# Kernel tuning notes

Measured on AMD Instinct MI355X. Metric: run time of the kernel, lower is better.

Reference implementation:

```python
import jax, jax.numpy as jnp
import numpy as np

NE, NT, NC, D, NR = 100000, 1024, 128, 128, 500
H, E, L_GCN = 8, 4, 2
B, DEG = 512, 8
NSRC = B * DEG
NNZ_E2T, NNZ_T2C, NNZ_E2C = 1000000, 50000, 500000
TAU, DECAY, CLW = 0.5, 1e-4, 0.1
N_NODES = NE + NT + NC


def setup_inputs() -> dict:
    ks = iter(jax.random.split(jax.random.key(0), 64))
    def n(shape, s=0.05):
        return jax.random.normal(next(ks), shape, jnp.float32) * s
    def ri(shape, hi):
        return jax.random.randint(next(ks), shape, 0, hi, jnp.int32)
    def u(shape):
        return jax.random.uniform(next(ks), shape, jnp.float32) * 0.01
    T = NT
    return {
        'entity_emb': n((NE, D)), 'type_emb': n((NT, D)), 'cluster_emb': n((NC, D)),
        'relation': n((NR, 2 * D)),
        'ln_g': jnp.ones((D,), jnp.float32), 'ln_b': jnp.zeros((D,), jnp.float32),
        'cl_w1': n((D, D)), 'cl_b1': jnp.zeros((D,), jnp.float32),
        'cl_w2': n((D, D)), 'cl_b2': jnp.zeros((D,), jnp.float32),
        'fc_w': n((2 * D, T)), 'fc_b': jnp.zeros((T,), jnp.float32),
        'wq': n((T, T)), 'bq': jnp.zeros((T,), jnp.float32),
        'wk': n((T, T)), 'bk': jnp.zeros((T,), jnp.float32),
        'wv': n((T, T)), 'bv': jnp.zeros((T,), jnp.float32),
        'wo': n((T, T)), 'bo': jnp.zeros((T,), jnp.float32),
        'gate_w': n((T, E)), 'exp_w': n((E, T, T)), 'exp_b': jnp.zeros((E, T), jnp.float32),
        'e2t_val': u((NNZ_E2T,)), 't2c_val': u((NNZ_T2C,)), 'e2c_val': u((NNZ_E2C,)),
        'e2t_row': ri((NNZ_E2T,), NE + NT), 'e2t_col': ri((NNZ_E2T,), NE + NT),
        't2c_row': ri((NNZ_T2C,), NT + NC), 't2c_col': ri((NNZ_T2C,), NT + NC),
        'e2c_row': ri((NNZ_E2C,), NE + NC), 'e2c_col': ri((NNZ_E2C,), NE + NC),
        'src_ids': ri((NSRC,), N_NODES), 'etype': ri((NSRC,), 2 * NR),
    }


def _light_gcn(ea, eb, row, col, val, na, nb):
    x = jnp.concatenate([ea, eb], axis=0)
    acc = x
    for _ in range(L_GCN):  # fixed small layer count
        x = jax.ops.segment_sum(val[:, None] * x[col], row, num_segments=na + nb)
        acc = acc + x
    m = acc / (L_GCN + 1)
    return m[:na], m[na:]


def _ln(x, g, b):
    mu = x.mean(-1, keepdims=True)
    var = x.var(-1, keepdims=True)
    return (x - mu) * jax.lax.rsqrt(var + 1e-5) * g + b


def _cl_loss(src1, src2, w1, b1, w2, b2):
    def proj(x):
        return jax.nn.elu(x @ w1 + b1) @ w2 + b2
    def norm(x):
        return x / jnp.maximum(jnp.linalg.norm(x, axis=1, keepdims=True), 1e-12)
    z1, z2 = norm(proj(src1)), norm(proj(src2))
    s11 = jnp.exp(z1 @ z1.T / TAU)   # [N,N]
    s12 = jnp.exp(z1 @ z2.T / TAU)
    s22 = jnp.exp(z2 @ z2.T / TAU)
    d12 = jnp.diag(s12)
    l1 = -jnp.log(d12 / (s11.sum(1) + s12.sum(1) - jnp.diag(s11)))
    l2 = -jnp.log(d12 / (s22.sum(1) + s12.sum(0) - jnp.diag(s22)))
    return ((l1 + l2) * 0.5).mean()


def _mha_moe(x, wq, bq, wk, bk, wv, bv, wo, bo, gate_w, exp_w, exp_b):
    # x: [B, DEG, T]; MHA over mailbox axis, then softmax-gated MoE, mean-pool.
    b, l, t = x.shape
    dh = t // H
    q = (x @ wq + bq).reshape(b, l, H, dh)
    k = (x @ wk + bk).reshape(b, l, H, dh)
    v = (x @ wv + bv).reshape(b, l, H, dh)
    attn = jax.nn.softmax(jnp.einsum('blhd,bmhd->bhlm', q, k) / jnp.sqrt(jnp.float32(dh)), axis=-1)
    o = jnp.einsum('bhlm,bmhd->blhd', attn, v).reshape(b, l, t) @ wo + bo
    gate = jax.nn.softmax(o @ gate_w, axis=-1)               # [B,L,E]
    eo = jnp.einsum('blt,etu->bleu', o, exp_w) + exp_b       # [B,L,E,T]
    moe = jnp.einsum('ble,blet->blt', gate, eo)
    return moe.mean(axis=1)                                  # [B,T]


def reference(entity_emb, type_emb, cluster_emb, relation, ln_g, ln_b,
              cl_w1, cl_b1, cl_w2, cl_b2, fc_w, fc_b,
              wq, bq, wk, bk, wv, bv, wo, bo, gate_w, exp_w, exp_b,
              e2t_val, t2c_val, e2c_val,
              e2t_row, e2t_col, t2c_row, t2c_col, e2c_row, e2c_col,
              src_ids, etype):
    e2t_e, e2t_t = _light_gcn(entity_emb, type_emb, e2t_row, e2t_col, e2t_val, NE, NT)
    t2c_t, t2c_c = _light_gcn(type_emb, cluster_emb, t2c_row, t2c_col, t2c_val, NT, NC)
    e2c_e, e2c_c = _light_gcn(entity_emb, cluster_emb, e2c_row, e2c_col, e2c_val, NE, NC)
    # with_norm=True path; dropout is eval-mode identity
    e2t_e, e2t_t = _ln(e2t_e, ln_g, ln_b), _ln(e2t_t, ln_g, ln_b)
    t2c_t, t2c_c = _ln(t2c_t, ln_g, ln_b), _ln(t2c_c, ln_g, ln_b)
    e2c_e, e2c_c = _ln(e2c_e, ln_g, ln_b), _ln(e2c_c, ln_g, ln_b)
    node1 = jnp.concatenate([e2t_e, e2t_t, t2c_c], axis=0)
    node2 = jnp.concatenate([e2c_e, t2c_t, e2c_c], axis=0)
    src1 = node1[src_ids]   # [NSRC, D]
    src2 = node2[src_ids]
    cl = _cl_loss(src1, src2, cl_w1, cl_b1, cl_w2, cl_b2)
    src = jnp.concatenate([src1, src2], axis=-1)  # [NSRC, 2D]
    sign = jnp.where(etype >= NR, -1.0, 1.0).astype(jnp.float32)[:, None]
    rel = relation[etype % NR] * sign
    emb_loss = DECAY * ((src ** 2).sum() + (rel ** 2).sum()) * 0.5 / rel.shape[0]
    aux_loss = CLW * cl + emb_loss
    # update_all: u_add_e message, regular mailbox [B, DEG, 2D]
    msg = jax.nn.relu(src + rel).reshape(B, DEG, 2 * D)
    predict = msg @ fc_w + fc_b                                  # [B, DEG, NT]
    predict = _mha_moe(predict, wq, bq, wk, bk, wv, bv, wo, bo, gate_w, exp_w, exp_b)
    out = jax.nn.sigmoid(predict)                                # [B, NT]
    return out, aux_loss
```

## Files before the change

### kernel.cpp

```cpp
#include <hip/hip_runtime.h>
#include <hip/hip_bf16.h>
#include <cmath>

constexpr int cNE = 100000, cNT = 1024, cNC = 128, cD = 128, cNR = 500;
constexpr int cB = 512, cNSRC = 4096, cT = 1024, cE = 4;
constexpr int cNNZ_E2T = 1000000, cNNZ_T2C = 50000, cNNZ_E2C = 500000;
constexpr float cDECAY = 1e-4f, cCLW = 0.1f;
constexpr int cNN_E2T = cNE + cNT;
constexpr int cNN_E2C = cNE + cNC;
constexpr int cNN_T2C = cNT + cNC;

constexpr size_t F_S1   = 0;
constexpr size_t F_S2   = F_S1 + 524288;
constexpr size_t F_PT   = F_S2 + 524288;
constexpr size_t F_Z1   = F_PT + 524288;
constexpr size_t F_Z2   = F_Z1 + 524288;
constexpr size_t F_MSG  = F_Z2 + 524288;
constexpr size_t F_GATE = F_MSG + 524288;
constexpr size_t F_SCAL = F_GATE + 16384;
constexpr size_t F_RS   = F_SCAL + 64;
constexpr size_t F_D11  = F_RS + 16384;
constexpr size_t F_D12  = F_D11 + 4096;
constexpr size_t F_D22  = F_D12 + 4096;
constexpr size_t F_U    = F_D22 + 4096;
constexpr size_t G_X1F  = F_U;
constexpr size_t G_X2C  = G_X1F + 6465536;
constexpr size_t G_SLOT = G_X2C + 262144;
constexpr size_t G_REP  = G_SLOT + 101376;
constexpr size_t G_RP   = G_REP + 4096;
constexpr size_t G_FILL = G_RP + 101376;
constexpr size_t G_COLS = G_FILL + 101376;
constexpr size_t G_VALS = G_COLS + 1000000;
constexpr size_t G_X1T  = G_VALS + 1000000;
constexpr size_t G_X2T  = G_X1T + 73728;
constexpr size_t G_BSUM = G_X2T + 73728;
constexpr size_t G_EBF  = G_BSUM + 512;
constexpr size_t G_TBF  = G_EBF + 3200000;
constexpr size_t G_CBF  = G_TBF + 65536;
constexpr size_t A_U0  = F_U;
constexpr size_t A_U1  = F_U + 2097152;
constexpr size_t A_WBT = F_U + 4 * 2097152;

typedef __attribute__((ext_vector_type(8))) short short8v;
typedef __attribute__((ext_vector_type(4))) float f32x4;

__device__ __forceinline__ void atomAdd(float* p, float v) {
  __hip_atomic_fetch_add(p, v, __ATOMIC_RELAXED, __HIP_MEMORY_SCOPE_AGENT);
}
__device__ __forceinline__ ushort f2bf(float f) {
  __hip_bfloat16 h = __float2bfloat16(f);
  return *reinterpret_cast<ushort*>(&h);
}
__device__ __forceinline__ float bf2f(ushort u) {
  __hip_bfloat16 h; *reinterpret_cast<ushort*>(&h) = u;
  return __bfloat162float(h);
}

__device__ __forceinline__ int mapNode(int mode, int id) {
  switch (mode) {
    case 0:  return (id < cNE + cNT) ? id : -1;
    case 1:  return (id >= cNE + cNT) ? (id - cNE) : -1;
    case 2:  return (id >= cNE && id < cNE + cNT) ? (id - cNE) : -1;
    default: return (id < cNE) ? id
                   : ((id >= cNE + cNT) ? (id - cNT) : -1);
  }
}

__device__ __forceinline__ float blockReduce256(float v, float* sh, int tid) {
  sh[tid] = v; __syncthreads();
  for (int s = 128; s > 0; s >>= 1) {
    if (tid < s) sh[tid] += sh[tid + s];
    __syncthreads();
  }
  float r = sh[0]; __syncthreads();
  return r;
}

__global__ __launch_bounds__(256) void k_to_bf(const float* __restrict__ src,
                                               ushort* __restrict__ dst, int nq) {
  for (int q = blockIdx.x * 256 + threadIdx.x; q < nq; q += gridDim.x * 256) {
    float4 v = *reinterpret_cast<const float4*>(src + (size_t)q * 4);
    ushort4 o;
    o.x = f2bf(v.x); o.y = f2bf(v.y); o.z = f2bf(v.z); o.w = f2bf(v.w);
    *reinterpret_cast<ushort4*>(dst + (size_t)q * 4) = o;
  }
}

__global__ __launch_bounds__(256) void k_pack_bias(const float* __restrict__ b0,
                                                   const float* __restrict__ b1,
                                                   const float* __restrict__ b2,
                                                   float* __restrict__ dst) {
  int i = blockIdx.x * 256 + threadIdx.x;
  float v = (i < 1024) ? b0[i] : (i < 2048) ? b1[i - 1024] : b2[i - 2048];
  dst[i] = v;
}

__global__ __launch_bounds__(256) void k_init3(int* __restrict__ slot, int* __restrict__ mark,
                                               int* __restrict__ fill, int n) {
  int i = blockIdx.x * 256 + threadIdx.x;
  if (i < n) { slot[i] = 0x7f7f7f7f; mark[i] = 0; fill[i] = 0; }
}

__global__ __launch_bounds__(256) void k_slot_mark(const int* __restrict__ ids,
                                                   int* __restrict__ slot,
                                                   int* __restrict__ mark, int mode) {
  int i = blockIdx.x * 256 + threadIdx.x;
  if (i >= cNSRC) return;
  int node = mapNode(mode, ids[i]);
  if (node >= 0) { atomicMin(&slot[node], i); mark[node] = 1; }
}

__global__ __launch_bounds__(256) void k_mark_edges(const int* __restrict__ row,
                                                    const int* __restrict__ col, int nnz,
                                                    const int* __restrict__ slot,
                                                    int* __restrict__ mark) {
  int e = blockIdx.x * 256 + threadIdx.x;
  if (e >= nnz) return;
  int r = row[e];
  if (slot[r] < cNSRC) mark[col[e]] = 1;
}

__global__ __launch_bounds__(256) void k_hist(const int* __restrict__ row, int nnz,
                                              const int* __restrict__ mark,
                                              int* __restrict__ cnt) {
  int e = blockIdx.x * 256 + threadIdx.x;
  if (e >= nnz) return;
  int r = row[e];
  if (mark && !mark[r]) return;
  atomicAdd(&cnt[r], 1);
}

__global__ __launch_bounds__(256) void k_scan_block(const int* __restrict__ cnt, int n,
                                                    int* __restrict__ excl, int* __restrict__ bsum) {
  __shared__ int sh[256];
  int tid = threadIdx.x;
  int i = blockIdx.x * 256 + tid;
  int v = (i < n) ? cnt[i] : 0;
  sh[tid] = v; __syncthreads();
  for (int off = 1; off < 256; off <<= 1) {
    int t = (tid >= off) ? sh[tid - off] : 0;
    __syncthreads();
    sh[tid] += t;
    __syncthreads();
  }
  if (i < n) excl[i] = sh[tid] - v;
  if (tid == 255) bsum[blockIdx.x] = sh[255];
}

__global__ __launch_bounds__(512) void k_bsum_scan(int* __restrict__ bsum, int nb,
                                                   int* __restrict__ rowptr, int n) {
  __shared__ int sh[512];
  int tid = threadIdx.x;
  int v = (tid < nb) ? bsum[tid] : 0;
  sh[tid] = v; __syncthreads();
  for (int off = 1; off < 512; off <<= 1) {
    int t = (tid >= off) ? sh[tid - off] : 0;
    __syncthreads();
    sh[tid] += t;
    __syncthreads();
  }
  if (tid < nb) bsum[tid] = sh[tid] - v;
  if (tid == 511) rowptr[n] = sh[511];
}

__global__ __launch_bounds__(256) void k_scan_add(int* __restrict__ rowptr,
                                                  const int* __restrict__ bsum, int n,
                                                  int* __restrict__ fill) {
  int i = blockIdx.x * 256 + threadIdx.x;
  if (i < n) {
    int r = rowptr[i] + bsum[blockIdx.x];
    rowptr[i] = r;
    fill[i] = r;
  }
}

__global__ __launch_bounds__(256) void k_fill(const int* __restrict__ row,
                                              const int* __restrict__ col,
                                              const float* __restrict__ val, int nnz,
                                              const int* __restrict__ mark,
                                              int* __restrict__ fill,
                                              int* __restrict__ cols, float* __restrict__ vals) {
  int e = blockIdx.x * 256 + threadIdx.x;
  if (e >= nnz) return;
  int r = row[e];
  if (mark && !mark[r]) return;
  int pos = atomicAdd(&fill[r], 1);
  cols[pos] = col[e];
  vals[pos] = val[e];
}

__global__ __launch_bounds__(256) void k_gather(
    const int* __restrict__ rowptr, const int* __restrict__ cols, const float* __restrict__ vals,
    const ushort* __restrict__ ea, const ushort* __restrict__ eb, int na,
    int nrows, const int* __restrict__ mark, ushort* __restrict__ out) {
  int r = blockIdx.x * 4 + (threadIdx.x >> 6);
  if (r >= nrows) return;
  if (mark && !mark[r]) return;
  int lane = threadIdx.x & 63;
  int p0 = rowptr[r], p1 = rowptr[r + 1];
  float ax = 0.f, ay = 0.f;
  int p = p0;
  for (; p + 4 <= p1; p += 4) {
    int c0 = cols[p], c1 = cols[p + 1], c2 = cols[p + 2], c3 = cols[p + 3];
    float v0 = vals[p], v1 = vals[p + 1], v2 = vals[p + 2], v3 = vals[p + 3];
    const ushort* s0 = (c0 < na) ? (ea + (size_t)c0 * cD) : (eb + (size_t)(c0 - na) * cD);
    const ushort* s1 = (c1 < na) ? (ea + (size_t)c1 * cD) : (eb + (size_t)(c1 - na) * cD);
    const ushort* s2 = (c2 < na) ? (ea + (size_t)c2 * cD) : (eb + (size_t)(c2 - na) * cD);
    const ushort* s3 = (c3 < na) ? (ea + (size_t)c3 * cD) : (eb + (size_t)(c3 - na) * cD);
    ushort2 x0 = *reinterpret_cast<const ushort2*>(s0 + lane * 2);
    ushort2 x1 = *reinterpret_cast<const ushort2*>(s1 + lane * 2);
    ushort2 x2 = *reinterpret_cast<const ushort2*>(s2 + lane * 2);
    ushort2 x3 = *reinterpret_cast<const ushort2*>(s3 + lane * 2);
    ax += v0 * bf2f(x0.x) + v1 * bf2f(x1.x) + v2 * bf2f(x2.x) + v3 * bf2f(x3.x);
    ay += v0 * bf2f(x0.y) + v1 * bf2f(x1.y) + v2 * bf2f(x2.y) + v3 * bf2f(x3.y);
  }
  for (; p < p1; ++p) {
    int c = cols[p];
    float v = vals[p];
    const ushort* s = (c < na) ? (ea + (size_t)c * cD) : (eb + (size_t)(c - na) * cD);
    ushort2 x = *reinterpret_cast<const ushort2*>(s + lane * 2);
    ax += v * bf2f(x.x); ay += v * bf2f(x.y);
  }
  ushort2 o; o.x = f2bf(ax); o.y = f2bf(ay);
  *reinterpret_cast<ushort2*>(out + (size_t)r * cD + lane * 2) = o;
}

__global__ __launch_bounds__(256) void k_rep(const int* __restrict__ ids,
                                             const int* __restrict__ slot, int mode,
                                             int* __restrict__ rep) {
  int i = blockIdx.x * 256 + threadIdx.x;
  if (i >= cNSRC) return;
  int node = mapNode(mode, ids[i]);
  rep[i] = (node >= 0 && slot[node] == i) ? node : -1;
}

__global__ __launch_bounds__(256) void k_gather_slot(
    const int* __restrict__ rowptr, const int* __restrict__ cols, const float* __restrict__ vals,
    const ushort* __restrict__ x1, const int* __restrict__ rep,
    ushort* __restrict__ outc) {
  int i = blockIdx.x * 4 + (threadIdx.x >> 6);
  if (i >= cNSRC) return;
  int r = rep[i];
  if (r < 0) return;
  int lane = threadIdx.x & 63;
  int p0 = rowptr[r], p1 = rowptr[r + 1];
  float ax = 0.f, ay = 0.f;
  int p = p0;
  for (; p + 4 <= p1; p += 4) {
    int c0 = cols[p], c1 = cols[p + 1], c2 = cols[p + 2], c3 = cols[p + 3];
    float v0 = vals[p], v1 = vals[p + 1], v2 = vals[p + 2], v3 = vals[p + 3];
    ushort2 x0 = *reinterpret_cast<const ushort2*>(x1 + (size_t)c0 * cD + lane * 2);
    ushort2 x1v = *reinterpret_cast<const ushort2*>(x1 + (size_t)c1 * cD + lane * 2);
    ushort2 x2 = *reinterpret_cast<const ushort2*>(x1 + (size_t)c2 * cD + lane * 2);
    ushort2 x3 = *reinterpret_cast<const ushort2*>(x1 + (size_t)c3 * cD + lane * 2);
    ax += v0 * bf2f(x0.x) + v1 * bf2f(x1v.x) + v2 * bf2f(x2.x) + v3 * bf2f(x3.x);
    ay += v0 * bf2f(x0.y) + v1 * bf2f(x1v.y) + v2 * bf2f(x2.y) + v3 * bf2f(x3.y);
  }
  for (; p < p1; ++p) {
    int c = cols[p];
    float v = vals[p];
    ushort2 x = *reinterpret_cast<const ushort2*>(x1 + (size_t)c * cD + lane * 2);
    ax += v * bf2f(x.x); ay += v * bf2f(x.y);
  }
  ushort2 o; o.x = f2bf(ax); o.y = f2bf(ay);
  *reinterpret_cast<ushort2*>(outc + (size_t)i * cD + lane * 2) = o;
}

__global__ __launch_bounds__(256) void k_gather_bf(
    const int* __restrict__ rowptr, const int* __restrict__ cols, const float* __restrict__ vals,
    const ushort* __restrict__ x1, int nrows, ushort* __restrict__ out) {
  int r = blockIdx.x * 4 + (threadIdx.x >> 6);
  if (r >= nrows) return;
  int lane = threadIdx.x & 63;
  int p0 = rowptr[r], p1 = rowptr[r + 1];
  float ax = 0.f, ay = 0.f;
  for (int p = p0; p < p1; ++p) {
    int c = cols[p];
    float v = vals[p];
    ushort2 x = *reinterpret_cast<const ushort2*>(x1 + (size_t)c * cD + lane * 2);
    ax += v * bf2f(x.x); ay += v * bf2f(x.y);
  }
  ushort2 o; o.x = f2bf(ax); o.y = f2bf(ay);
  *reinterpret_cast<ushort2*>(out + (size_t)r * cD + lane * 2) = o;
}

__global__ __launch_bounds__(128) void gather_ln(
    const int* __restrict__ ids, int mode,
    const float* __restrict__ ea, const float* __restrict__ eb, int na,
    const ushort* __restrict__ x1, const ushort* __restrict__ x2, const int* __restrict__ slot,
    const float* __restrict__ g, const float* __restrict__ bia, float* __restrict__ dst) {
  __shared__ float shx[2], shy[2];
  int i = blockIdx.x;
  int tid = threadIdx.x;
  int id = ids[i];
  int node = mapNode(mode, id);
  if (node < 0) return;
  const float* x0 = (node < na) ? (ea + (size_t)node * cD) : (eb + (size_t)(node - na) * cD);
  int xi2 = slot ? slot[node] : node;
  float a = (x0[tid] + bf2f(x1[(size_t)node * cD + tid]) + bf2f(x2[(size_t)xi2 * cD + tid]))
            * (1.0f / 3.0f);
  float sx = a, sy = a * a;
#pragma unroll
  for (int off = 32; off > 0; off >>= 1) {
    sx += __shfl_xor(sx, off);
    sy += __shfl_xor(sy, off);
  }
  if ((tid & 63) == 0) { shx[tid >> 6] = sx; shy[tid >> 6] = sy; }
  __syncthreads();
  float s  = shx[0] + shx[1];
  float ss = shy[0] + shy[1];
  float mu = s * (1.0f / 128.0f);
  float var = ss * (1.0f / 128.0f) - mu * mu;
  float y = (a - mu) * rsqrtf(var + 1e-5f) * g[tid] + bia[tid];
  dst[(size_t)i * cD + tid] = y;
}

__global__ __launch_bounds__(256) void gemm_bf(
    const ushort* __restrict__ A, const ushort* __restrict__ Bt,
    int N, int K, const float* __restrict__ bias, ushort* __restrict__ Cbf, int epi) {
  __shared__ ushort As[128 * 40];
  __shared__ ushort Bs[128 * 40];
  const int bx = blockIdx.x, by = blockIdx.y;
  const int t = threadIdx.x;
  const int wv = t >> 6, lane = t & 63;
  const int wr = (wv >> 1) * 64, wc = (wv & 1) * 64;
  const int srow = t >> 1, shalf = t & 1;
  const ushort* Ag = A + (size_t)(by * 128 + srow) * K + shalf * 16;
  const ushort* Bg = Bt + (size_t)(bx * 128 + srow) * K + shalf * 16;
  uint4 ra0 = *reinterpret_cast<const uint4*>(Ag);
  uint4 ra1 = *reinterpret_cast<const uint4*>(Ag + 8);
  uint4 rb0 = *reinterpret_cast<const uint4*>(Bg);
  uint4 rb1 = *reinterpret_cast<const uint4*>(Bg + 8);
  f32x4 acc[4][4];
  const f32x4 z4 = {0.f, 0.f, 0.f, 0.f};
#pragma unroll
  for (int i = 0; i < 4; ++i)
#pragma unroll
    for (int j = 0; j < 4; ++j) acc[i][j] = z4;
  const int la = lane & 15, lk = (lane >> 4) * 8;
  const int sdst = srow * 40 + shalf * 16;
  for (int kt = 0; kt < K; kt += 32) {
    __syncthreads();
    *reinterpret_cast<uint4*>(&As[sdst])     = ra0;
    *reinterpret_cast<uint4*>(&As[sdst + 8]) = ra1;
    *reinterpret_cast<uint4*>(&Bs[sdst])     = rb0;
    *reinterpret_cast<uint4*>(&Bs[sdst + 8]) = rb1;
    __syncthreads();
    if (kt + 32 < K) {
      ra0 = *reinterpret_cast<const uint4*>(Ag + kt + 32);
      ra1 = *reinterpret_cast<const uint4*>(Ag + kt + 40);
      rb0 = *reinterpret_cast<const uint4*>(Bg + kt + 32);
      rb1 = *reinterpret_cast<const uint4*>(Bg + kt + 40);
    }
    short8v af[4], bfr[4];
#pragma unroll
    for (int i = 0; i < 4; ++i)
      af[i] = *reinterpret_cast<const short8v*>(&As[(wr + i * 16 + la) * 40 + lk]);
#pragma unroll
    for (int j = 0; j < 4; ++j)
      bfr[j] = *reinterpret_cast<const short8v*>(&Bs[(wc + j * 16 + la) * 40 + lk]);
#pragma unroll
    for (int i = 0; i < 4; ++i)
#pragma unroll
      for (int j = 0; j < 4; ++j)
        acc[i][j] = __builtin_amdgcn_mfma_f32_16x16x32_bf16(af[i], bfr[j], acc[i][j], 0, 0, 0);
  }
  const int r0 = by * 128 + wr + (lane >> 4) * 4;
  const int c0 = bx * 128 + wc + la;
#pragma unroll
  for (int i = 0; i < 4; ++i)
#pragma unroll
    for (int j = 0; j < 4; ++j) {
      int c = c0 + j * 16;
      float bv = bias[c];
#pragma unroll
      for (int q = 0; q < 4; ++q) {
        int r = r0 + i * 16 + q;
        float v = acc[i][j][q] + bv;
        if (epi == 1) v = (v > 0.0f) ? v : expm1f(v);
        Cbf[(size_t)r * N + c] = f2bf(v);
      }
    }
}

__global__ __launch_bounds__(256) void k_gate_pool(
    const ushort* __restrict__ o, const float* __restrict__ gw,
    ushort* __restrict__ ae, float* __restrict__ gsum) {
  __shared__ float os[8][1024];
  __shared__ float lg[8][4];
  __shared__ float gs[8][4];
  const int b = blockIdx.x, t = threadIdx.x;
  for (int u = t; u < 8192; u += 256) {
    int l = u >> 10, d = u & 1023;
    os[l][d] = bf2f(o[(size_t)(b * 8 + l) * 1024 + d]);
  }
  __syncthreads();
  {
    int p = t >> 3, sub = t & 7;
    int l = p >> 2, e = p & 3;
    float s = 0;
    for (int d = sub; d < 1024; d += 8) s += os[l][d] * gw[d * 4 + e];
    s += __shfl_down(s, 4, 8);
    s += __shfl_down(s, 2, 8);
    s += __shfl_down(s, 1, 8);
    if (sub == 0) lg[l][e] = s;
  }
  __syncthreads();
  if (t < 8) {
    float m = fmaxf(fmaxf(lg[t][0], lg[t][1]), fmaxf(lg[t][2], lg[t][3]));
    float e0 = expf(lg[t][0] - m), e1 = expf(lg[t][1] - m);
    float e2 = expf(lg[t][2] - m), e3 = expf(lg[t][3] - m);
    float inv = 1.0f / (e0 + e1 + e2 + e3);
    gs[t][0] = e0 * inv; gs[t][1] = e1 * inv;
    gs[t][2] = e2 * inv; gs[t][3] = e3 * inv;
  }
  __syncthreads();
  if (t < 4) {
    float g = 0;
#pragma unroll
    for (int l = 0; l < 8; ++l) g += gs[l][t];
    gsum[b * 4 + t] = g;
  }
#pragma unroll
  for (int rep = 0; rep < 4; ++rep) {
    int d = t + rep * 256;
    float a0 = 0, a1 = 0, a2 = 0, a3 = 0;
#pragma unroll
    for (int l = 0; l < 8; ++l) {
      float ov = os[l][d];
      a0 += gs[l][0] * ov; a1 += gs[l][1] * ov;
      a2 += gs[l][2] * ov; a3 += gs[l][3] * ov;
    }
    ae[(size_t)0 * 524288 + b * 1024 + d] = f2bf(a0);
    ae[(size_t)1 * 524288 + b * 1024 + d] = f2bf(a1);
    ae[(size_t)2 * 524288 + b * 1024 + d] = f2bf(a2);
    ae[(size_t)3 * 524288 + b * 1024 + d] = f2bf(a3);
  }
}

__global__ __launch_bounds__(256) void gemm_moe2(
    const ushort* __restrict__ AE, const ushort* __restrict__ Bt4,
    const float* __restrict__ expb, const float* __restrict__ gsum,
    float* __restrict__ out) {
  __shared__ ushort As[64 * 40];
  __shared__ ushort Bs[64 * 40];
  const int bx = blockIdx.x, by = blockIdx.y;
  const int t = threadIdx.x;
  const int wv = t >> 6, lane = t & 63;
  const int wr = (wv >> 1) * 32, wc = (wv & 1) * 32;
  const int srow = t >> 2, sq = t & 3;
  const int la = lane & 15, lk = (lane >> 4) * 8;
  const int sdst = srow * 40 + sq * 8;
// ... 206 lines not shown
  int tx = threadIdx.x & 31, ty = threadIdx.x >> 5;
#pragma unroll
  for (int i = 0; i < 4; ++i)
    tile[ty + 8 * i][tx] = W[(size_t)(k0 + ty + 8 * i) * N + n0 + tx];
  __syncthreads();
#pragma unroll
  for (int i = 0; i < 4; ++i)
    Bt[(size_t)(n0 + ty + 8 * i) * K + k0 + tx] = f2bf(tile[tx][ty + 8 * i]);
}

__global__ __launch_bounds__(256) void k_post_s(
    const float* __restrict__ s1, const float* __restrict__ s2,
    const float* __restrict__ relation, const int* __restrict__ etype,
    ushort* __restrict__ sb, ushort* __restrict__ msg, float* __restrict__ emb_out) {
  __shared__ float sh[256];
  float part = 0.f;
  for (int idx = blockIdx.x * 256 + threadIdx.x; idx < 1048576; idx += 128 * 256) {
    float vs = (idx < 524288) ? s1[idx] : s2[idx - 524288];
    sb[idx] = f2bf(vs);
    int i = idx >> 8, j = idx & 255;
    int et = etype[i];
    float sign = (et >= cNR) ? -1.0f : 1.0f;
    float r = relation[(size_t)(et % cNR) * 256 + j];
    float s = (j < 128) ? s1[(size_t)i * 128 + j] : s2[(size_t)i * 128 + j - 128];
    msg[idx] = f2bf(fmaxf(s + r * sign, 0.0f));
    part += s * s + r * r;
  }
  float tot = blockReduce256(part, sh, threadIdx.x);
  if (threadIdx.x == 0) atomAdd(emb_out, tot);
}

__global__ __launch_bounds__(128) void rownorm_bf2(ushort* __restrict__ w) {
  __shared__ float sh[2];
  int i = blockIdx.x, tid = threadIdx.x;
  float v = bf2f(w[(size_t)i * cD + tid]);
  float ss = v * v;
#pragma unroll
  for (int off = 32; off > 0; off >>= 1) ss += __shfl_xor(ss, off);
  if ((tid & 63) == 0) sh[tid >> 6] = ss;
  __syncthreads();
  float n = fmaxf(sqrtf(sh[0] + sh[1]), 1e-12f);
  w[(size_t)i * cD + tid] = f2bf(v / n);
}

__global__ __launch_bounds__(64) void mha_attn(
    const ushort* __restrict__ qkv, ushort* __restrict__ o) {
  __shared__ float qs[8][132], ks[8][132], vs[8][132];
  __shared__ float att[8][8];
  int bh = blockIdx.x;
  int b = bh >> 3, h = bh & 7;
  int tid = threadIdx.x;
  for (int u = tid; u < 256; u += 64) {
    int l = u >> 5;
    int d4 = (u & 31) * 4;
    size_t base = (size_t)(b * 8 + l) * 3072 + h * 128 + d4;
    ushort4 qv = *reinterpret_cast<const ushort4*>(qkv + base);
    ushort4 kv = *reinterpret_cast<const ushort4*>(qkv + base + 1024);
    ushort4 vv = *reinterpret_cast<const ushort4*>(qkv + base + 2048);
    qs[l][d4] = bf2f(qv.x); qs[l][d4 + 1] = bf2f(qv.y);
    qs[l][d4 + 2] = bf2f(qv.z); qs[l][d4 + 3] = bf2f(qv.w);
    ks[l][d4] = bf2f(kv.x); ks[l][d4 + 1] = bf2f(kv.y);
    ks[l][d4 + 2] = bf2f(kv.z); ks[l][d4 + 3] = bf2f(kv.w);
    vs[l][d4] = bf2f(vv.x); vs[l][d4 + 1] = bf2f(vv.y);
    vs[l][d4 + 2] = bf2f(vv.z); vs[l][d4 + 3] = bf2f(vv.w);
  }
  __syncthreads();
  int l = tid >> 3, m = tid & 7;
  const float4* qp = reinterpret_cast<const float4*>(&qs[l][0]);
  const float4* kp = reinterpret_cast<const float4*>(&ks[m][0]);
  float s = 0;
#pragma unroll
  for (int d4 = 0; d4 < 32; ++d4) {
    float4 a = qp[d4], bb = kp[d4];
    s += a.x * bb.x + a.y * bb.y + a.z * bb.z + a.w * bb.w;
  }
  s *= 0.08838834764831845f;
  float mx = s;
  for (int off = 1; off < 8; off <<= 1) mx = fmaxf(mx, __shfl_xor(mx, off, 8));
  float p = expf(s - mx);
  float sum = p;
  for (int off = 1; off < 8; off <<= 1) sum += __shfl_xor(sum, off, 8);
  att[l][m] = p / sum;
  __syncthreads();
  for (int u = tid; u < 1024; u += 64) {
    int ll = u >> 7, d = u & 127;
    float acc = 0;
#pragma unroll
    for (int mm = 0; mm < 8; ++mm) acc += att[ll][mm] * vs[mm][d];
    o[(size_t)(b * 8 + ll) * 1024 + h * 128 + d] = f2bf(acc);
  }
}

__global__ void finalize_k(const float* __restrict__ scal, float* __restrict__ out_aux) {
  float cl = scal[0] * (1.0f / cNSRC);
  float emb = cDECAY * 0.5f * scal[1] * (1.0f / cNSRC);
  out_aux[0] = cCLW * cl + emb;
}

extern "C" void kernel_launch(void* const* d_in, const int* in_sizes, int n_in,
                              void* d_out, int out_size, void* d_ws, size_t ws_size,
                              hipStream_t stream) {
  (void)in_sizes; (void)n_in; (void)out_size; (void)ws_size;
  const float* entity   = (const float*)d_in[0];
  const float* type_e   = (const float*)d_in[1];
  const float* cluster  = (const float*)d_in[2];
  const float* relation = (const float*)d_in[3];
  const float* ln_g  = (const float*)d_in[4];
  const float* ln_b  = (const float*)d_in[5];
  const float* cl_w1 = (const float*)d_in[6];
  const float* cl_b1 = (const float*)d_in[7];
  const float* cl_w2 = (const float*)d_in[8];
  const float* cl_b2 = (const float*)d_in[9];
  const float* fc_w  = (const float*)d_in[10];
  const float* fc_b  = (const float*)d_in[11];
  const float* wq = (const float*)d_in[12];
  const float* bq = (const float*)d_in[13];
  const float* wk = (const float*)d_in[14];
  const float* bk = (const float*)d_in[15];
  const float* wv = (const float*)d_in[16];
  const float* bv = (const float*)d_in[17];
  const float* wo = (const float*)d_in[18];
  const float* bo = (const float*)d_in[19];
  const float* gate_w = (const float*)d_in[20];
  const float* exp_w  = (const float*)d_in[21];
  const float* exp_b  = (const float*)d_in[22];
  const float* e2t_val = (const float*)d_in[23];
  const float* t2c_val = (const float*)d_in[24];
  const float* e2c_val = (const float*)d_in[25];
  const int* e2t_row = (const int*)d_in[26];
  const int* e2t_col = (const int*)d_in[27];
  const int* t2c_row = (const int*)d_in[28];
  const int* t2c_col = (const int*)d_in[29];
  const int* e2c_row = (const int*)d_in[30];
  const int* e2c_col = (const int*)d_in[31];
  const int* src_ids = (const int*)d_in[32];
  const int* etype   = (const int*)d_in[33];

  float* ws = (float*)d_ws;
  float* S1 = ws + F_S1;
  float* S2 = ws + F_S2;
  ushort* Wbf = (ushort*)(ws + F_PT);
  ushort* P1bf = (ushort*)(ws + F_Z1);
  ushort* SBbf = (ushort*)(ws + F_Z2);
  ushort* MSGbf = (ushort*)(ws + F_MSG);
  float* GSUM = ws + F_GATE;
  float* SCAL = ws + F_SCAL;
  float* RS   = ws + F_RS;
  float* BQKV = ws + F_GATE + 8192;
  float* D11  = ws + F_D11;
  float* D12  = ws + F_D12;
  float* D22  = ws + F_D22;
  ushort* X1F = (ushort*)(ws + G_X1F);
  ushort* X2C = (ushort*)(ws + G_X2C);
  int*   MARK = (int*)(ws + G_X2C);
  int*   SLOT = (int*)(ws + G_SLOT);
  int*   REP  = (int*)(ws + G_REP);
  int*   RP   = (int*)(ws + G_RP);
  int*   FILL = (int*)(ws + G_FILL);
  int*   COLS = (int*)(ws + G_COLS);
  float* VALS = ws + G_VALS;
  ushort* X1T = (ushort*)(ws + G_X1T);
  ushort* X2T = (ushort*)(ws + G_X2T);
  int*   BSUM = (int*)(ws + G_BSUM);
  ushort* EBF = (ushort*)(ws + G_EBF);
  ushort* TBF = (ushort*)(ws + G_TBF);
  ushort* CBF = (ushort*)(ws + G_CBF);
  ushort* PB   = (ushort*)(ws + A_U0);
  ushort* AE   = (ushort*)(ws + A_U0);
  ushort* QKV  = (ushort*)(ws + A_U1);
  ushort* OB   = (ushort*)(ws + A_U1);
  ushort* WBT  = (ushort*)(ws + A_WBT);

  hipMemsetAsync(SCAL, 0, 2 * sizeof(float), stream);
  hipMemsetAsync(RS, 0, (16384 + 3 * 4096) * sizeof(float), stream);

  k_to_bf<<<2048, 256, 0, stream>>>(entity, EBF, cNE * cD / 4);
  k_to_bf<<<128, 256, 0, stream>>>(type_e, TBF, cNT * cD / 4);
  k_to_bf<<<16, 256, 0, stream>>>(cluster, CBF, cNC * cD / 4);

  auto run_gcn_masked = [&](const int* row, const int* col, const float* val, int nnz, int nn,
                            const float* ea_f, const float* eb_f,
                            const ushort* ea_b, const ushort* eb_b, int na, int mode,
                            float* dst) {
    int nb = (nn + 255) / 256;
    int gEdge = (nnz + 255) / 256;
    k_init3<<<nb, 256, 0, stream>>>(SLOT, MARK, FILL, nn);
    k_slot_mark<<<16, 256, 0, stream>>>(src_ids, SLOT, MARK, mode);
    k_mark_edges<<<gEdge, 256, 0, stream>>>(row, col, nnz, SLOT, MARK);
    k_hist<<<gEdge, 256, 0, stream>>>(row, nnz, MARK, FILL);
    k_scan_block<<<nb, 256, 0, stream>>>(FILL, nn, RP, BSUM);
    k_bsum_scan<<<1, 512, 0, stream>>>(BSUM, nb, RP, nn);
    k_scan_add<<<nb, 256, 0, stream>>>(RP, BSUM, nn, FILL);
    k_fill<<<gEdge, 256, 0, stream>>>(row, col, val, nnz, MARK, FILL, COLS, VALS);
    k_rep<<<16, 256, 0, stream>>>(src_ids, SLOT, mode, REP);
    k_gather<<<(nn + 3) / 4, 256, 0, stream>>>(RP, COLS, VALS, ea_b, eb_b, na, nn, MARK, X1F);
    k_gather_slot<<<cNSRC / 4, 256, 0, stream>>>(RP, COLS, VALS, X1F, REP, X2C);
    gather_ln<<<cNSRC, 128, 0, stream>>>(src_ids, mode, ea_f, eb_f, na, X1F, X2C, SLOT,
                                         ln_g, ln_b, dst);
  };

  run_gcn_masked(e2t_row, e2t_col, e2t_val, cNNZ_E2T, cNN_E2T,
                 entity, type_e, EBF, TBF, cNE, 0, S1);
  run_gcn_masked(e2c_row, e2c_col, e2c_val, cNNZ_E2C, cNN_E2C,
                 entity, cluster, EBF, CBF, cNE, 3, S2);

  {
    int nn = cNN_T2C, nb = (nn + 255) / 256, gEdge = (cNNZ_T2C + 255) / 256;
    hipMemsetAsync(FILL, 0, (size_t)nn * sizeof(int), stream);
    k_hist<<<gEdge, 256, 0, stream>>>(t2c_row, cNNZ_T2C, nullptr, FILL);
    k_scan_block<<<nb, 256, 0, stream>>>(FILL, nn, RP, BSUM);
    k_bsum_scan<<<1, 512, 0, stream>>>(BSUM, nb, RP, nn);
    k_scan_add<<<nb, 256, 0, stream>>>(RP, BSUM, nn, FILL);
    k_fill<<<gEdge, 256, 0, stream>>>(t2c_row, t2c_col, t2c_val, cNNZ_T2C, nullptr,
                                      FILL, COLS, VALS);
    k_gather<<<(nn + 3) / 4, 256, 0, stream>>>(RP, COLS, VALS, TBF, CBF, cNT,
                                               nn, nullptr, X1T);
    k_gather_bf<<<(nn + 3) / 4, 256, 0, stream>>>(RP, COLS, VALS, X1T, nn, X2T);
    gather_ln<<<cNSRC, 128, 0, stream>>>(src_ids, 1, type_e, cluster, cNT, X1T, X2T, nullptr,
                                         ln_g, ln_b, S1);
    gather_ln<<<cNSRC, 128, 0, stream>>>(src_ids, 2, type_e, cluster, cNT, X1T, X2T, nullptr,
                                         ln_g, ln_b, S2);
  }

  k_post_s<<<128, 256, 0, stream>>>(S1, S2, relation, etype, SBbf, MSGbf, SCAL + 1);

  ushort* W1T = WBT;
  ushort* W2T = WBT + 16384;
  k_wt_bt<<<dim3(4, 4), 256, 0, stream>>>(cl_w1, W1T, cD, cD);
  k_wt_bt<<<dim3(4, 4), 256, 0, stream>>>(cl_w2, W2T, cD, cD);
  gemm_bf<<<dim3(1, 64), 256, 0, stream>>>(SBbf, W1T, cD, cD, cl_b1, P1bf, 1);
  gemm_bf<<<dim3(1, 64), 256, 0, stream>>>(P1bf, W2T, cD, cD, cl_b2, Wbf, 0);
  rownorm_bf2<<<2 * cNSRC, 128, 0, stream>>>(Wbf);
  gram_sym<<<2080, 256, 0, stream>>>(Wbf, RS, D11, D12, D22);
  cl_row<<<16, 256, 0, stream>>>(RS, D11, D12, D22, SCAL);

  k_wt_bt<<<dim3(cT / 32, 256 / 32), 256, 0, stream>>>(fc_w, WBT, 256, cT);
  gemm_bf<<<dim3(cT / 128, cNSRC / 128), 256, 0, stream>>>(MSGbf, WBT, cT, 256, fc_b, PB, 0);

  k_wt_bt4<<<dim3(32, 32, 4), 256, 0, stream>>>(wq, wk, wv, wo, WBT, cT, cT);
  k_pack_bias<<<12, 256, 0, stream>>>(bq, bk, bv, BQKV);
  gemm_bf<<<dim3(3072 / 128, cNSRC / 128), 256, 0, stream>>>(PB, WBT, 3072, cT, BQKV, QKV, 0);
  mha_attn<<<cB * 8, 64, 0, stream>>>(QKV, PB);
  gemm_bf<<<dim3(cT / 128, cNSRC / 128), 256, 0, stream>>>(PB, WBT + 3 * 1048576, cT, cT,
                                                           bo, OB, 0);

  k_gate_pool<<<cB, 256, 0, stream>>>(OB, gate_w, AE, GSUM);
  k_wt_bt_s<<<dim3(32, 32, 4), 256, 0, stream>>>(exp_w, WBT, cT, cT);
  gemm_moe2<<<dim3(16, 8), 256, 0, stream>>>(AE, WBT, exp_b, GSUM, (float*)d_out);

  finalize_k<<<1, 1, 0, stream>>>(SCAL, (float*)d_out + (size_t)cB * cT);
}
```

Baseline: 528.5 us.

## Batch CSR construction for all three graphs into grid-z fused launches

After: 490.8 us. -7.1%, faster.

```diff
diff --git a/kernel.cpp b/kernel.cpp
--- a/kernel.cpp
+++ b/kernel.cpp
@@ -9,6 +9,9 @@
 constexpr int cNN_E2T = cNE + cNT;
 constexpr int cNN_E2C = cNE + cNC;
 constexpr int cNN_T2C = cNT + cNC;
+constexpr int SL_STR = 101376;
+constexpr int RP_STR = 101400;
+constexpr int CO_E2T = 0, CO_E2C = 1000000, CO_T2C = 1500000;
 
 constexpr size_t F_S1   = 0;
 constexpr size_t F_S2   = F_S1 + 524288;
@@ -26,15 +29,16 @@
 constexpr size_t G_X1F  = F_U;
 constexpr size_t G_X2C  = G_X1F + 6465536;
 constexpr size_t G_SLOT = G_X2C + 262144;
-constexpr size_t G_REP  = G_SLOT + 101376;
-constexpr size_t G_RP   = G_REP + 4096;
-constexpr size_t G_FILL = G_RP + 101376;
-constexpr size_t G_COLS = G_FILL + 101376;
-constexpr size_t G_VALS = G_COLS + 1000000;
-constexpr size_t G_X1T  = G_VALS + 1000000;
+constexpr size_t G_MARK = G_SLOT + 202752;
+constexpr size_t G_REP  = G_MARK + 202752;
+constexpr size_t G_RP   = G_REP + 8192;
+constexpr size_t G_FILL = G_RP + 304200;
+constexpr size_t G_BSUM = G_FILL + 304128;
+constexpr size_t G_COLS = G_BSUM + 1536;
+constexpr size_t G_VALS = G_COLS + 1550000;
+constexpr size_t G_X1T  = G_VALS + 1550000;
 constexpr size_t G_X2T  = G_X1T + 73728;
-constexpr size_t G_BSUM = G_X2T + 73728;
-constexpr size_t G_EBF  = G_BSUM + 512;
+constexpr size_t G_EBF  = G_X2T + 73728;
 constexpr size_t G_TBF  = G_EBF + 3200000;
 constexpr size_t G_CBF  = G_TBF + 65536;
 constexpr size_t A_U0  = F_U;
@@ -76,13 +80,21 @@
   return r;
 }
 
-__global__ __launch_bounds__(256) void k_to_bf(const float* __restrict__ src,
-                                               ushort* __restrict__ dst, int nq) {
-  for (int q = blockIdx.x * 256 + threadIdx.x; q < nq; q += gridDim.x * 256) {
-    float4 v = *reinterpret_cast<const float4*>(src + (size_t)q * 4);
+__global__ __launch_bounds__(256) void k_to_bf3(
+    const float* __restrict__ se, const float* __restrict__ st, const float* __restrict__ sc,
+    ushort* __restrict__ de, ushort* __restrict__ dt, ushort* __restrict__ dc) {
+  constexpr int NQE = cNE * cD / 4;
+  constexpr int NQT = cNT * cD / 4;
+  constexpr int NQC = cNC * cD / 4;
+  for (int q = blockIdx.x * 256 + threadIdx.x; q < NQE + NQT + NQC; q += gridDim.x * 256) {
+    const float* src; ushort* dst; int qq;
+    if (q < NQE)            { src = se; dst = de; qq = q; }
+    else if (q < NQE + NQT) { src = st; dst = dt; qq = q - NQE; }
+    else                    { src = sc; dst = dc; qq = q - NQE - NQT; }
+    float4 v = *reinterpret_cast<const float4*>(src + (size_t)qq * 4);
     ushort4 o;
     o.x = f2bf(v.x); o.y = f2bf(v.y); o.z = f2bf(v.z); o.w = f2bf(v.w);
-    *reinterpret_cast<ushort4*>(dst + (size_t)q * 4) = o;
+    *reinterpret_cast<ushort4*>(dst + (size_t)qq * 4) = o;
   }
 }
 
@@ -95,47 +107,68 @@
   dst[i] = v;
 }
 
-__global__ __launch_bounds__(256) void k_init3(int* __restrict__ slot, int* __restrict__ mark,
-                                               int* __restrict__ fill, int n) {
+__global__ __launch_bounds__(256) void k_csr_init3(int* __restrict__ slotb,
+                                                   int* __restrict__ markb,
+                                                   int* __restrict__ fillb) {
+  const int nn3[3] = {cNN_E2T, cNN_E2C, cNN_T2C};
+  int z = blockIdx.z;
   int i = blockIdx.x * 256 + threadIdx.x;
-  if (i < n) { slot[i] = 0x7f7f7f7f; mark[i] = 0; fill[i] = 0; }
-}
-
-__global__ __launch_bounds__(256) void k_slot_mark(const int* __restrict__ ids,
-                                                   int* __restrict__ slot,
-                                                   int* __restrict__ mark, int mode) {
+  if (i >= nn3[z]) return;
+  fillb[z * SL_STR + i] = 0;
+  if (z < 2) {
+    slotb[z * SL_STR + i] = 0x7f7f7f7f;
+    markb[z * SL_STR + i] = 0;
+  }
+}
+
+__global__ __launch_bounds__(256) void k_slot_mark2(const int* __restrict__ ids,
+                                                    int* __restrict__ slotb,
+                                                    int* __restrict__ markb) {
+  int z = blockIdx.z;
+  int mode = z ? 3 : 0;
   int i = blockIdx.x * 256 + threadIdx.x;
   if (i >= cNSRC) return;
   int node = mapNode(mode, ids[i]);
-  if (node >= 0) { atomicMin(&slot[node], i); mark[node] = 1; }
-}
-
-__global__ __launch_bounds__(256) void k_mark_edges(const int* __restrict__ row,
-                                                    const int* __restrict__ col, int nnz,
-                                                    const int* __restrict__ slot,
-                                                    int* __restrict__ mark) {
+  if (node >= 0) { atomicMin(&slotb[z * SL_STR + node], i); markb[z * SL_STR + node] = 1; }
+}
+
+__global__ __launch_bounds__(256) void k_mark_edges2(
+    const int* __restrict__ r0, const int* __restrict__ c0,
+    const int* __restrict__ r1, const int* __restrict__ c1,
+    const int* __restrict__ slotb, int* __restrict__ markb) {
+  int z = blockIdx.z;
+  int nnzv = z ? cNNZ_E2C : cNNZ_E2T;
   int e = blockIdx.x * 256 + threadIdx.x;
-  if (e >= nnz) return;
+  if (e >= nnzv) return;
+  const int* row = z ? r1 : r0;
+  const int* col = z ? c1 : c0;
   int r = row[e];
-  if (slot[r] < cNSRC) mark[col[e]] = 1;
-}
-
-__global__ __launch_bounds__(256) void k_hist(const int* __restrict__ row, int nnz,
-                                              const int* __restrict__ mark,
-                                              int* __restrict__ cnt) {
+  if (slotb[z * SL_STR + r] < cNSRC) markb[z * SL_STR + col[e]] = 1;
+}
+
+__global__ __launch_bounds__(256) void k_hist3(
+    const int* __restrict__ r0, const int* __restrict__ r1, const int* __restrict__ r2,
+    const int* __restrict__ markb, int* __restrict__ fillb) {
+  const int nnz3[3] = {cNNZ_E2T, cNNZ_E2C, cNNZ_T2C};
+  int z = blockIdx.z;
   int e = blockIdx.x * 256 + threadIdx.x;
-  if (e >= nnz) return;
+  if (e >= nnz3[z]) return;
+  const int* row = (z == 0) ? r0 : (z == 1) ? r1 : r2;
   int r = row[e];
-  if (mark && !mark[r]) return;
-  atomicAdd(&cnt[r], 1);
-}
-
-__global__ __launch_bounds__(256) void k_scan_block(const int* __restrict__ cnt, int n,
-                                                    int* __restrict__ excl, int* __restrict__ bsum) {
+  if (z < 2 && !markb[z * SL_STR + r]) return;
+  atomicAdd(&fillb[z * SL_STR + r], 1);
+}
+
+__global__ __launch_bounds__(256) void k_scan_block3(const int* __restrict__ fillb,
+                                                     int* __restrict__ rpb,
+                                                     int* __restrict__ bsumb) {
   __shared__ int sh[256];
+  const int nn3[3] = {cNN_E2T, cNN_E2C, cNN_T2C};
+  int z = blockIdx.z;
+  int n = nn3[z];
   int tid = threadIdx.x;
   int i = blockIdx.x * 256 + tid;
-  int v = (i < n) ? cnt[i] : 0;
+  int v = (i < n) ? fillb[z * SL_STR + i] : 0;
   sh[tid] = v; __syncthreads();
   for (int off = 1; off < 256; off <<= 1) {
     int t = (tid >= off) ? sh[tid - off] : 0;
@@ -143,15 +176,18 @@
     sh[tid] += t;
     __syncthreads();
   }
-  if (i < n) excl[i] = sh[tid] - v;
-  if (tid == 255) bsum[blockIdx.x] = sh[255];
-}
-
-__global__ __launch_bounds__(512) void k_bsum_scan(int* __restrict__ bsum, int nb,
-                                                   int* __restrict__ rowptr, int n) {
+  if (i < n) rpb[z * RP_STR + i] = sh[tid] - v;
+  if (tid == 255) bsumb[z * 512 + blockIdx.x] = sh[255];
+}
+
+__global__ __launch_bounds__(512) void k_bsum_scan3(int* __restrict__ bsumb,
+                                                    int* __restrict__ rpb) {
   __shared__ int sh[512];
+  const int nn3[3] = {cNN_E2T, cNN_E2C, cNN_T2C};
+  int z = blockIdx.x;
+  int n = nn3[z];
   int tid = threadIdx.x;
-  int v = (tid < nb) ? bsum[tid] : 0;
+  int v = (tid < 396) ? bsumb[z * 512 + tid] : 0;
   sh[tid] = v; __syncthreads();
   for (int off = 1; off < 512; off <<= 1) {
     int t = (tid >= off) ? sh[tid - off] : 0;
@@ -159,34 +195,53 @@
     sh[tid] += t;
     __syncthreads();
   }
-  if (tid < nb) bsum[tid] = sh[tid] - v;
-  if (tid == 511) rowptr[n] = sh[511];
-}
-
-__global__ __launch_bounds__(256) void k_scan_add(int* __restrict__ rowptr,
-                                                  const int* __restrict__ bsum, int n,
-                                                  int* __restrict__ fill) {
+  if (tid < 396) bsumb[z * 512 + tid] = sh[tid] - v;
+  if (tid == 511) rpb[z * RP_STR + n] = sh[511];
+}
+
+__global__ __launch_bounds__(256) void k_scan_add3(int* __restrict__ rpb,
+                                                   const int* __restrict__ bsumb,
+                                                   int* __restrict__ fillb) {
+  const int nn3[3] = {cNN_E2T, cNN_E2C, cNN_T2C};
+  int z = blockIdx.z;
   int i = blockIdx.x * 256 + threadIdx.x;
-  if (i < n) {
-    int r = rowptr[i] + bsum[blockIdx.x];
-    rowptr[i] = r;
-    fill[i] = r;
-  }
-}
-
-__global__ __launch_bounds__(256) void k_fill(const int* __restrict__ row,
-                                              const int* __restrict__ col,
-                                              const float* __restrict__ val, int nnz,
-                                              const int* __restrict__ mark,
-                                              int* __restrict__ fill,
-                                              int* __restrict__ cols, float* __restrict__ vals) {
+  if (i < nn3[z]) {
+    int r = rpb[z * RP_STR + i] + bsumb[z * 512 + blockIdx.x];
+    rpb[z * RP_STR + i] = r;
+    fillb[z * SL_STR + i] = r;
+  }
+}
+
+__global__ __launch_bounds__(256) void k_fill3(
+    const int* __restrict__ r0, const int* __restrict__ c0, const float* __restrict__ v0,
+    const int* __restrict__ r1, const int* __restrict__ c1, const float* __restrict__ v1,
+    const int* __restrict__ r2, const int* __restrict__ c2, const float* __restrict__ v2,
+    const int* __restrict__ markb, int* __restrict__ fillb,
+    int* __restrict__ colsb, float* __restrict__ valsb) {
+  const int nnz3[3] = {cNNZ_E2T, cNNZ_E2C, cNNZ_T2C};
+  const int coff[3] = {CO_E2T, CO_E2C, CO_T2C};
+  int z = blockIdx.z;
   int e = blockIdx.x * 256 + threadIdx.x;
-  if (e >= nnz) return;
+  if (e >= nnz3[z]) return;
+  const int* row = (z == 0) ? r0 : (z == 1) ? r1 : r2;
+  const int* col = (z == 0) ? c0 : (z == 1) ? c1 : c2;
+  const float* val = (z == 0) ? v0 : (z == 1) ? v1 : v2;
   int r = row[e];
-  if (mark && !mark[r]) return;
-  int pos = atomicAdd(&fill[r], 1);
-  cols[pos] = col[e];
-  vals[pos] = val[e];
+  if (z < 2 && !markb[z * SL_STR + r]) return;
+  int pos = atomicAdd(&fillb[z * SL_STR + r], 1);
+  colsb[coff[z] + pos] = col[e];
+  valsb[coff[z] + pos] = val[e];
+}
+
+__global__ __launch_bounds__(256) void k_rep2(const int* __restrict__ ids,
+                                              const int* __restrict__ slotb,
+                                              int* __restrict__ repb) {
+  int z = blockIdx.z;
+  int mode = z ? 3 : 0;
+  int i = blockIdx.x * 256 + threadIdx.x;
+  if (i >= cNSRC) return;
+  int node = mapNode(mode, ids[i]);
+  repb[z * 4096 + i] = (node >= 0 && slotb[z * SL_STR + node] == i) ? node : -1;
 }
 
 __global__ __launch_bounds__(256) void k_gather(
@@ -225,15 +280,6 @@
   *reinterpret_cast<ushort2*>(out + (size_t)r * cD + lane * 2) = o;
 }
 
-__global__ __launch_bounds__(256) void k_rep(const int* __restrict__ ids,
-                                             const int* __restrict__ slot, int mode,
-                                             int* __restrict__ rep) {
-  int i = blockIdx.x * 256 + threadIdx.x;
-  if (i >= cNSRC) return;
-  int node = mapNode(mode, ids[i]);
-  rep[i] = (node >= 0 && slot[node] == i) ? node : -1;
-}
-
 __global__ __launch_bounds__(256) void k_gather_slot(
     const int* __restrict__ rowptr, const int* __restrict__ cols, const float* __restrict__ vals,
     const ushort* __restrict__ x1, const int* __restrict__ rep,
@@ -298,6 +344,41 @@
   const float* x0 = (node < na) ? (ea + (size_t)node * cD) : (eb + (size_t)(node - na) * cD);
   int xi2 = slot ? slot[node] : node;
   float a = (x0[tid] + bf2f(x1[(size_t)node * cD + tid]) + bf2f(x2[(size_t)xi2 * cD + tid]))
+            * (1.0f / 3.0f);
+  float sx = a, sy = a * a;
+#pragma unroll
+  for (int off = 32; off > 0; off >>= 1) {
+    sx += __shfl_xor(sx, off);
+    sy += __shfl_xor(sy, off);
+  }
+  if ((tid & 63) == 0) { shx[tid >> 6] = sx; shy[tid >> 6] = sy; }
+  __syncthreads();
+  float s  = shx[0] + shx[1];
+  float ss = shy[0] + shy[1];
+  float mu = s * (1.0f / 128.0f);
+  float var = ss * (1.0f / 128.0f) - mu * mu;
+  float y = (a - mu) * rsqrtf(var + 1e-5f) * g[tid] + bia[tid];
+  dst[(size_t)i * cD + tid] = y;
+}
+
+__global__ __launch_bounds__(128) void gather_ln_t2(
+    const int* __restrict__ ids,
+    const float* __restrict__ type_e, const float* __restrict__ cluster,
+    const ushort* __restrict__ x1, const ushort* __restrict__ x2,
+    const float* __restrict__ g, const float* __restrict__ bia,
+    float* __restrict__ s1, float* __restrict__ s2) {
+  __shared__ float shx[2], shy[2];
+  int z = blockIdx.y;
+  int mode = z ? 2 : 1;
+  float* dst = z ? s2 : s1;
+  int i = blockIdx.x;
+  int tid = threadIdx.x;
+  int id = ids[i];
+  int node = mapNode(mode, id);
+  if (node < 0) return;
+  const float* x0 = (node < cNT) ? (type_e + (size_t)node * cD)
+                                 : (cluster + (size_t)(node - cNT) * cD);
+  float a = (x0[tid] + bf2f(x1[(size_t)node * cD + tid]) + bf2f(x2[(size_t)node * cD + tid]))
             * (1.0f / 3.0f);
   float sx = a, sy = a * a;
 #pragma unroll
@@ -810,16 +891,16 @@
   float* D22  = ws + F_D22;
   ushort* X1F = (ushort*)(ws + G_X1F);
   ushort* X2C = (ushort*)(ws + G_X2C);
-  int*   MARK = (int*)(ws + G_X2C);
-  int*   SLOT = (int*)(ws + G_SLOT);
-  int*   REP  = (int*)(ws + G_REP);
-  int*   RP   = (int*)(ws + G_RP);
-  int*   FILL = (int*)(ws + G_FILL);
-  int*   COLS = (int*)(ws + G_COLS);
-  float* VALS = ws + G_VALS;
+  int*   SLOTb = (int*)(ws + G_SLOT);
+  int*   MARKb = (int*)(ws + G_MARK);
+  int*   REPb  = (int*)(ws + G_REP);
+  int*   RPb   = (int*)(ws + G_RP);
+  int*   FILLb = (int*)(ws + G_FILL);
+  int*   BSUMb = (int*)(ws + G_BSUM);
+  int*   COLSb = (int*)(ws + G_COLS);
+  float* VALSb = ws + G_VALS;
   ushort* X1T = (ushort*)(ws + G_X1T);
   ushort* X2T = (ushort*)(ws + G_X2T);
-  int*   BSUM = (int*)(ws + G_BSUM);
   ushort* EBF = (ushort*)(ws + G_EBF);
   ushort* TBF = (ushort*)(ws + G_TBF);
   ushort* CBF = (ushort*)(ws + G_CBF);
@@ -832,53 +913,46 @@
   hipMemsetAsync(SCAL, 0, 2 * sizeof(float), stream);
   hipMemsetAsync(RS, 0, (16384 + 3 * 4096) * sizeof(float), stream);
 
-  k_to_bf<<<2048, 256, 0, stream>>>(entity, EBF, cNE * cD / 4);
-  k_to_bf<<<128, 256, 0, stream>>>(type_e, TBF, cNT * cD / 4);
-  k_to_bf<<<16, 256, 0, stream>>>(cluster, CBF, cNC * cD / 4);
-
-  auto run_gcn_masked = [&](const int* row, const int* col, const float* val, int nnz, int nn,
-                            const float* ea_f, const float* eb_f,
-                            const ushort* ea_b, const ushort* eb_b, int na, int mode,
-                            float* dst) {
-    int nb = (nn + 255) / 256;
-    int gEdge = (nnz + 255) / 256;
-    k_init3<<<nb, 256, 0, stream>>>(SLOT, MARK, FILL, nn);
-    k_slot_mark<<<16, 256, 0, stream>>>(src_ids, SLOT, MARK, mode);
-    k_mark_edges<<<gEdge, 256, 0, stream>>>(row, col, nnz, SLOT, MARK);
-    k_hist<<<gEdge, 256, 0, stream>>>(row, nnz, MARK, FILL);
-    k_scan_block<<<nb, 256, 0, stream>>>(FILL, nn, RP, BSUM);
-    k_bsum_scan<<<1, 512, 0, stream>>>(BSUM, nb, RP, nn);
-    k_scan_add<<<nb, 256, 0, stream>>>(RP, BSUM, nn, FILL);
-    k_fill<<<gEdge, 256, 0, stream>>>(row, col, val, nnz, MARK, FILL, COLS, VALS);
-    k_rep<<<16, 256, 0, stream>>>(src_ids, SLOT, mode, REP);
-    k_gather<<<(nn + 3) / 4, 256, 0, stream>>>(RP, COLS, VALS, ea_b, eb_b, na, nn, MARK, X1F);
-    k_gather_slot<<<cNSRC / 4, 256, 0, stream>>>(RP, COLS, VALS, X1F, REP, X2C);
-    gather_ln<<<cNSRC, 128, 0, stream>>>(src_ids, mode, ea_f, eb_f, na, X1F, X2C, SLOT,
-                                         ln_g, ln_b, dst);
-  };
-
-  run_gcn_masked(e2t_row, e2t_col, e2t_val, cNNZ_E2T, cNN_E2T,
-                 entity, type_e, EBF, TBF, cNE, 0, S1);
-  run_gcn_masked(e2c_row, e2c_col, e2c_val, cNNZ_E2C, cNN_E2C,
-                 entity, cluster, EBF, CBF, cNE, 3, S2);
-
-  {
-    int nn = cNN_T2C, nb = (nn + 255) / 256, gEdge = (cNNZ_T2C + 255) / 256;
-    hipMemsetAsync(FILL, 0, (size_t)nn * sizeof(int), stream);
-    k_hist<<<gEdge, 256, 0, stream>>>(t2c_row, cNNZ_T2C, nullptr, FILL);
-    k_scan_block<<<nb, 256, 0, stream>>>(FILL, nn, RP, BSUM);
-    k_bsum_scan<<<1, 512, 0, stream>>>(BSUM, nb, RP, nn);
-    k_scan_add<<<nb, 256, 0, stream>>>(RP, BSUM, nn, FILL);
-    k_fill<<<gEdge, 256, 0, stream>>>(t2c_row, t2c_col, t2c_val, cNNZ_T2C, nullptr,
-                                      FILL, COLS, VALS);
-    k_gather<<<(nn + 3) / 4, 256, 0, stream>>>(RP, COLS, VALS, TBF, CBF, cNT,
-                                               nn, nullptr, X1T);
-    k_gather_bf<<<(nn + 3) / 4, 256, 0, stream>>>(RP, COLS, VALS, X1T, nn, X2T);
-    gather_ln<<<cNSRC, 128, 0, stream>>>(src_ids, 1, type_e, cluster, cNT, X1T, X2T, nullptr,
-                                         ln_g, ln_b, S1);
-    gather_ln<<<cNSRC, 128, 0, stream>>>(src_ids, 2, type_e, cluster, cNT, X1T, X2T, nullptr,
-                                         ln_g, ln_b, S2);
-  }
+  k_to_bf3<<<2048, 256, 0, stream>>>(entity, type_e, cluster, EBF, TBF, CBF);
+
+  const int gEdgeMax = (cNNZ_E2T + 255) / 256;
+  const int nbMax = 396;
+  k_csr_init3<<<dim3(nbMax, 1, 3), 256, 0, stream>>>(SLOTb, MARKb, FILLb);
+  k_slot_mark2<<<dim3(16, 1, 2), 256, 0, stream>>>(src_ids, SLOTb, MARKb);
+  k_mark_edges2<<<dim3(gEdgeMax, 1, 2), 256, 0, stream>>>(e2t_row, e2t_col,
+                                                          e2c_row, e2c_col, SLOTb, MARKb);
+  k_hist3<<<dim3(gEdgeMax, 1, 3), 256, 0, stream>>>(e2t_row, e2c_row, t2c_row, MARKb, FILLb);
+  k_scan_block3<<<dim3(nbMax, 1, 3), 256, 0, stream>>>(FILLb, RPb, BSUMb);
+  k_bsum_scan3<<<3, 512, 0, stream>>>(BSUMb, RPb);
+  k_scan_add3<<<dim3(nbMax, 1, 3), 256, 0, stream>>>(RPb, BSUMb, FILLb);
+  k_fill3<<<dim3(gEdgeMax, 1, 3), 256, 0, stream>>>(e2t_row, e2t_col, e2t_val,
+                                                    e2c_row, e2c_col, e2c_val,
+                                                    t2c_row, t2c_col, t2c_val,
+                                                    MARKb, FILLb, COLSb, VALSb);
+  k_rep2<<<dim3(16, 1, 2), 256, 0, stream>>>(src_ids, SLOTb, REPb);
+
+  k_gather<<<(cNN_E2T + 3) / 4, 256, 0, stream>>>(RPb, COLSb + CO_E2T, VALSb + CO_E2T,
+                                                  EBF, TBF, cNE, cNN_E2T, MARKb, X1F);
+  k_gather_slot<<<cNSRC / 4, 256, 0, stream>>>(RPb, COLSb + CO_E2T, VALSb + CO_E2T,
+                                               X1F, REPb, X2C);
+  gather_ln<<<cNSRC, 128, 0, stream>>>(src_ids, 0, entity, type_e, cNE, X1F, X2C, SLOTb,
+                                       ln_g, ln_b, S1);
+
+  k_gather<<<(cNN_E2C + 3) / 4, 256, 0, stream>>>(RPb + RP_STR, COLSb + CO_E2C, VALSb + CO_E2C,
+                                                  EBF, CBF, cNE, cNN_E2C,
+                                                  MARKb + SL_STR, X1F);
+  k_gather_slot<<<cNSRC / 4, 256, 0, stream>>>(RPb + RP_STR, COLSb + CO_E2C, VALSb + CO_E2C,
+                                               X1F, REPb + 4096, X2C);
+  gather_ln<<<cNSRC, 128, 0, stream>>>(src_ids, 3, entity, cluster, cNE, X1F, X2C,
+                                       SLOTb + SL_STR, ln_g, ln_b, S2);
+
+  k_gather<<<(cNN_T2C + 3) / 4, 256, 0, stream>>>(RPb + 2 * RP_STR, COLSb + CO_T2C,
+                                                  VALSb + CO_T2C, TBF, CBF, cNT,
+                                                  cNN_T2C, nullptr, X1T);
+  k_gather_bf<<<(cNN_T2C + 3) / 4, 256, 0, stream>>>(RPb + 2 * RP_STR, COLSb + CO_T2C,
+                                                     VALSb + CO_T2C, X1T, cNN_T2C, X2T);
+  gather_ln_t2<<<dim3(cNSRC, 2), 128, 0, stream>>>(src_ids, type_e, cluster, X1T, X2T,
+                                                   ln_g, ln_b, S1, S2);
 
   k_post_s<<<128, 256, 0, stream>>>(S1, S2, relation, etype, SBbf, MSGbf, SCAL + 1);
 
```
